# Kernel optimization log

Measured on AMD Instinct MI355X. Metric: run time of the kernel, lower is better.

Reference implementation:

```python
import jax, jax.numpy as jnp
import numpy as np

N, D = 2048, 1024
OUT = 65536
S = 16384  # number of LSH-selected neurons


def setup_inputs() -> dict:
    key = jax.random.key(0)
    k1, k2, k3, k4 = jax.random.split(key, 4)
    x = jax.random.normal(k1, (N, D), dtype=jnp.float32)
    # original init: uniform(-1, 1) weights, zero bias; use randn-scale weights per spec
    weight = jax.random.normal(k2, (OUT, D), dtype=jnp.float32)
    bias = jax.random.normal(k3, (OUT,), dtype=jnp.float32)
    sample_ids = jax.random.randint(k4, (S,), 0, OUT, dtype=jnp.int64)
    return {"x": x, "weight": weight, "bias": bias, "sample_ids": sample_ids}


def reference(x, weight, bias, sample_ids):
    # Gather selected neuron rows (F.embedding equivalent)
    sample_weights = weight[sample_ids]          # [S, D]
    sample_bias = bias[sample_ids]               # [S]
    # x @ W_sel.T + b_sel  -> [N, S]
    sample_logits = jnp.einsum('nd,sd->ns', x, sample_weights) + sample_bias
    return sample_logits
```

## Files before the change

kernel.cpp:

```cpp
#include <hip/hip_runtime.h>
#include <stdint.h>


typedef __bf16 bf16x8 __attribute__((ext_vector_type(8)));
typedef float f32x4 __attribute__((ext_vector_type(4)));

#define BM 128
#define BN 128
#define BK 64

__device__ __forceinline__ ushort f2bf(float f) {
  union { float f; uint32_t u; } c; c.f = f;
  uint32_t u = c.u;
  return (ushort)((u + 0x7FFFu + ((u >> 16) & 1u)) >> 16);
}

__global__ void convert_x_kernel(const float* __restrict__ x,
                                 ushort* __restrict__ xb) {
  int i = blockIdx.x * blockDim.x + threadIdx.x;
  float4 v = ((const float4*)x)[i];
  ushort4 o;
  o.x = f2bf(v.x); o.y = f2bf(v.y); o.z = f2bf(v.z); o.w = f2bf(v.w);
  ((ushort4*)xb)[i] = o;
}

__global__ void gather_kernel(const float* __restrict__ W,
                              const float* __restrict__ bias,
                              const int* __restrict__ ids,
                              ushort* __restrict__ Wg,
                              float* __restrict__ biasg,
                              int D) {
  int s = blockIdx.x;
  int id = ids[s];
  const float4* src = (const float4*)(W + (size_t)id * D);
  ushort4* dst = (ushort4*)(Wg + (size_t)s * D);
  int t = threadIdx.x;
  float4 v = src[t];
  ushort4 o;
  o.x = f2bf(v.x); o.y = f2bf(v.y); o.z = f2bf(v.z); o.w = f2bf(v.w);
  dst[t] = o;
  if (t == 0) biasg[s] = bias[id];
}

__device__ __forceinline__ void load_lds16(const void* g, void* l) {
  __builtin_amdgcn_global_load_lds(
      (const __attribute__((address_space(1))) void*)g,
      (__attribute__((address_space(3))) void*)l, 16, 0, 0);
}

__global__ __launch_bounds__(256) void gemm_bt_bias(
    const ushort* __restrict__ A, const ushort* __restrict__ B,
    const float* __restrict__ biasg, float* __restrict__ C,
    int M, int S, int K) {
  __shared__ __align__(16) ushort As[BM * BK];
  __shared__ __align__(16) ushort Bs[BN * BK];

  const int tid  = threadIdx.x;
  const int lane = tid & 63;
  const int wave = tid >> 6;
  const int bn = blockIdx.x;
  const int bm = blockIdx.y;

  const int wm = (wave >> 1) * 64;
  const int wn = (wave & 1) * 64;
  const int quad = lane >> 4;
  const int l16  = lane & 15;

  const int srow = tid >> 3;
  const int scol = (tid & 7) * 8;
  const ushort* Ag = A + (size_t)(bm * BM + srow) * K + scol;
  const ushort* Bg = B + (size_t)(bn * BN + srow) * K + scol;
  ushort* Asl = As + tid * 8;
  ushort* Bsl = Bs + tid * 8;

  f32x4 acc[4][4] = {};

  for (int kt = 0; kt < K; kt += BK) {
#pragma unroll
    for (int i = 0; i < 4; ++i) {
      load_lds16(Ag + (size_t)(i * 32) * K, Asl + i * 32 * BK);
      load_lds16(Bg + (size_t)(i * 32) * K, Bsl + i * 32 * BK);
    }
    Ag += BK; Bg += BK;
    __syncthreads();

#pragma unroll
    for (int ks = 0; ks < BK; ks += 32) {
      bf16x8 af[4], bq[4];
#pragma unroll
      for (int i = 0; i < 4; ++i)
        af[i] = *(const bf16x8*)(As + (wm + i * 16 + l16) * BK + ks + quad * 8);
#pragma unroll
      for (int j = 0; j < 4; ++j)
        bq[j] = *(const bf16x8*)(Bs + (wn + j * 16 + l16) * BK + ks + quad * 8);
#pragma unroll
      for (int i = 0; i < 4; ++i)
#pragma unroll
        for (int j = 0; j < 4; ++j)
          acc[i][j] = __builtin_amdgcn_mfma_f32_16x16x32_bf16(
              af[i], bq[j], acc[i][j], 0, 0, 0);
    }
    __syncthreads();
  }

  const int row0 = bm * BM + wm + quad * 4;
  const int col0 = bn * BN + wn + l16;
#pragma unroll
  for (int j = 0; j < 4; ++j) {
    const int col = col0 + j * 16;
    const float bv = biasg[col];
#pragma unroll
    for (int i = 0; i < 4; ++i) {
#pragma unroll
      for (int r = 0; r < 4; ++r) {
        C[(size_t)(row0 + i * 16 + r) * S + col] = acc[i][j][r] + bv;
      }
    }
  }
}

extern "C" void kernel_launch(void* const* d_in, const int* in_sizes, int n_in,
                              void* d_out, int out_size, void* d_ws, size_t ws_size,
                              hipStream_t stream) {
  const float* x    = (const float*)d_in[0];
  const float* W    = (const float*)d_in[1];
  const float* bias = (const float*)d_in[2];
  const int*   ids  = (const int*)d_in[3];
  float* out = (float*)d_out;

  const int OUTN = in_sizes[2];
  const int S    = in_sizes[3];
  const int D    = in_sizes[1] / OUTN;
  const int N    = in_sizes[0] / D;

  ushort* Wg = (ushort*)d_ws;
  ushort* xb = (ushort*)((char*)d_ws + (size_t)S * D * sizeof(ushort));
  float* biasg = (float*)((char*)d_ws + (size_t)S * D * sizeof(ushort)
                          + (size_t)N * D * sizeof(ushort));

  convert_x_kernel<<<(N * D / 4 + 255) / 256, 256, 0, stream>>>(x, xb);
  gather_kernel<<<S, D / 4, 0, stream>>>(W, bias, ids, Wg, biasg, D);

  dim3 grid(S / BN, N / BM);
  gemm_bt_bias<<<grid, 256, 0, stream>>>(xb, Wg, biasg, out, N, S, D);
}
```

Measured before the change: 450.6 us.

## Swizzle LDS tiles to avoid bank conflicts and merge prep kernels

The GEMM's LDS layout gets an XOR swizzle: each 16-byte chunk column is XORed with the row index on the global->LDS load side and on the fragment read side. This targets bank conflicts on the ds_read of bf16x8 fragments, where all rows share a 128-byte stride. Separately, the x conversion and the weight gather/convert are merged into one launch, with each gather block handling 8 rows. That saves one kernel launch at the cost of a slightly more branchy prep kernel.

Measured after the change: 433.2 us. -3.9%, faster.

```diff
diff --git a/kernel.cpp b/kernel.cpp
--- a/kernel.cpp
+++ b/kernel.cpp
@@ -15,37 +15,43 @@
   return (ushort)((u + 0x7FFFu + ((u >> 16) & 1u)) >> 16);
 }
 
-__global__ void convert_x_kernel(const float* __restrict__ x,
-                                 ushort* __restrict__ xb) {
-  int i = blockIdx.x * blockDim.x + threadIdx.x;
-  float4 v = ((const float4*)x)[i];
-  ushort4 o;
-  o.x = f2bf(v.x); o.y = f2bf(v.y); o.z = f2bf(v.z); o.w = f2bf(v.w);
-  ((ushort4*)xb)[i] = o;
-}
-
-__global__ void gather_kernel(const float* __restrict__ W,
-                              const float* __restrict__ bias,
-                              const int* __restrict__ ids,
-                              ushort* __restrict__ Wg,
-                              float* __restrict__ biasg,
-                              int D) {
-  int s = blockIdx.x;
-  int id = ids[s];
-  const float4* src = (const float4*)(W + (size_t)id * D);
-  ushort4* dst = (ushort4*)(Wg + (size_t)s * D);
-  int t = threadIdx.x;
-  float4 v = src[t];
-  ushort4 o;
-  o.x = f2bf(v.x); o.y = f2bf(v.y); o.z = f2bf(v.z); o.w = f2bf(v.w);
-  dst[t] = o;
-  if (t == 0) biasg[s] = bias[id];
+__global__ __launch_bounds__(256) void prep_kernel(
+    const float* __restrict__ x, const float* __restrict__ W,
+    const float* __restrict__ bias, const int* __restrict__ ids,
+    ushort* __restrict__ Wg, ushort* __restrict__ xb,
+    float* __restrict__ biasg, int D, int S) {
+  const int t = threadIdx.x;
+  const int gblocks = S >> 3;
+  if ((int)blockIdx.x < gblocks) {
+    const int s0 = blockIdx.x << 3;
+    if (t < 8) biasg[s0 + t] = bias[ids[s0 + t]];
+#pragma unroll
+    for (int r = 0; r < 8; ++r) {
+      const int s = s0 + r;
+      const int id = ids[s];
+      float4 v = ((const float4*)(W + (size_t)id * D))[t];
+      ushort4 o;
+      o.x = f2bf(v.x); o.y = f2bf(v.y); o.z = f2bf(v.z); o.w = f2bf(v.w);
+      ((ushort4*)(Wg + (size_t)s * D))[t] = o;
+    }
+  } else {
+    const int i = (blockIdx.x - gblocks) * 256 + t;
+    float4 v = ((const float4*)x)[i];
+    ushort4 o;
+    o.x = f2bf(v.x); o.y = f2bf(v.y); o.z = f2bf(v.z); o.w = f2bf(v.w);
+    ((ushort4*)xb)[i] = o;
+  }
 }
 
 __device__ __forceinline__ void load_lds16(const void* g, void* l) {
   __builtin_amdgcn_global_load_lds(
       (const __attribute__((address_space(1))) void*)g,
       (__attribute__((address_space(3))) void*)l, 16, 0, 0);
+}
+
+__device__ __forceinline__ const ushort* frag_ptr(const ushort* base, int row,
+                                                  int c) {
+  return base + row * BK + (((c ^ (row & 7)) << 3));
 }
 
 __global__ __launch_bounds__(256) void gemm_bt_bias(
@@ -67,7 +73,7 @@
   const int l16  = lane & 15;
 
   const int srow = tid >> 3;
-  const int scol = (tid & 7) * 8;
+  const int scol = (((tid & 7) ^ (srow & 7)) << 3);
   const ushort* Ag = A + (size_t)(bm * BM + srow) * K + scol;
   const ushort* Bg = B + (size_t)(bn * BN + srow) * K + scol;
   ushort* Asl = As + tid * 8;
@@ -86,13 +92,14 @@
 
 #pragma unroll
     for (int ks = 0; ks < BK; ks += 32) {
+      const int c0 = (ks >> 3) + quad;
       bf16x8 af[4], bq[4];
 #pragma unroll
       for (int i = 0; i < 4; ++i)
-        af[i] = *(const bf16x8*)(As + (wm + i * 16 + l16) * BK + ks + quad * 8);
+        af[i] = *(const bf16x8*)frag_ptr(As, wm + i * 16 + l16, c0);
 #pragma unroll
       for (int j = 0; j < 4; ++j)
-        bq[j] = *(const bf16x8*)(Bs + (wn + j * 16 + l16) * BK + ks + quad * 8);
+        bq[j] = *(const bf16x8*)frag_ptr(Bs, wn + j * 16 + l16, c0);
 #pragma unroll
       for (int i = 0; i < 4; ++i)
 #pragma unroll
@@ -138,8 +145,10 @@
   float* biasg = (float*)((char*)d_ws + (size_t)S * D * sizeof(ushort)
                           + (size_t)N * D * sizeof(ushort));
 
-  convert_x_kernel<<<(N * D / 4 + 255) / 256, 256, 0, stream>>>(x, xb);
-  gather_kernel<<<S, D / 4, 0, stream>>>(W, bias, ids, Wg, biasg, D);
+  const int gather_blocks = S / 8;
+  const int conv_blocks = (N * D) / 1024;
+  prep_kernel<<<gather_blocks + conv_blocks, 256, 0, stream>>>(
+      x, W, bias, ids, Wg, xb, biasg, D, S);
 
   dim3 grid(S / BN, N / BM);
   gemm_bt_bias<<<grid, 256, 0, stream>>>(xb, Wg, biasg, out, N, S, D);
```
